# Kernel tuning notes

Hardware: AMD Instinct MI355X
Metric: run time of the kernel (lower is better)

The kernel has to match this reference:

```python
import jax, jax.numpy as jnp
import numpy as np

PAD = 1
K = 3  # kernel_size


def conv2d(x, w, b):
    y = jax.lax.conv_general_dilated(
        x, w, window_strides=(1, 1), padding=((PAD, PAD), (PAD, PAD)),
        dimension_numbers=("NCHW", "OIHW", "NCHW"))
    return y + b[None, :, None, None]


def deform_conv2d(x, offset, weight, bias):
    # torchvision.ops.deform_conv2d semantics (stride=1, dilation=1, 1 offset group)
    B, C, H, W = x.shape
    O = weight.shape[0]
    K2 = K * K
    off = offset.reshape(B, K2, 2, H, W)  # [...,0]=dy, [...,1]=dx
    ky, kx = jnp.meshgrid(jnp.arange(K), jnp.arange(K), indexing="ij")
    ky = ky.reshape(K2).astype(x.dtype)
    kx = kx.reshape(K2).astype(x.dtype)
    hh = jnp.arange(H, dtype=x.dtype)
    ww = jnp.arange(W, dtype=x.dtype)
    # sampling coords, shape [B, K2, H, W]
    py = off[:, :, 0] + ky[None, :, None, None] + hh[None, None, :, None] - PAD
    px = off[:, :, 1] + kx[None, :, None, None] + ww[None, None, None, :] - PAD

    y0 = jnp.floor(py)
    x0 = jnp.floor(px)
    wy = (py - y0)[:, None]  # [B,1,K2,H,W]
    wx = (px - x0)[:, None]

    xf = x.reshape(B, C, H * W)

    def gather(iy, ix):
        valid = (iy >= 0) & (iy < H) & (ix >= 0) & (ix < W)
        iyc = jnp.clip(iy, 0, H - 1).astype(jnp.int32)
        ixc = jnp.clip(ix, 0, W - 1).astype(jnp.int32)
        idx = (iyc * W + ixc).reshape(B, 1, K2 * H * W)
        v = jnp.take_along_axis(xf, idx, axis=2).reshape(B, C, K2, H, W)
        return v * valid.reshape(B, 1, K2, H, W).astype(x.dtype)

    v00 = gather(y0, x0)
    v01 = gather(y0, x0 + 1)
    v10 = gather(y0 + 1, x0)
    v11 = gather(y0 + 1, x0 + 1)
    sampled = (v00 * (1 - wy) * (1 - wx) + v01 * (1 - wy) * wx
               + v10 * wy * (1 - wx) + v11 * wy * wx)  # [B,C,K2,H,W]
    out = jnp.einsum("bckhw,ock->bohw", sampled, weight.reshape(O, C, K2))
    return out + bias[None, :, None, None]


def setup_inputs() -> dict:
    key = jax.random.key(0)
    k1, k2, k3, k4, k5 = jax.random.split(key, 5)
    B, C, H, W = 4, 64, 192, 192
    O = 64
    x = jax.random.normal(k1, (B, C, H, W), dtype=jnp.float32)
    w_off = jax.random.normal(k2, (2 * K * K, C, K, K), dtype=jnp.float32) * 0.05
    b_off = jnp.zeros((2 * K * K,), dtype=jnp.float32)
    w_conv = jax.random.normal(k3, (O, C, K, K), dtype=jnp.float32) * (1.0 / np.sqrt(C * K * K))
    b_conv = jax.random.normal(k4, (O,), dtype=jnp.float32) * 0.01
    return {"x": x, "w_off": w_off, "b_off": b_off, "w_conv": w_conv, "b_conv": b_conv}


def reference(x, w_off, b_off, w_conv, b_conv):
    offset = conv2d(x, w_off, b_off)
    y = deform_conv2d(x, offset, w_conv, b_conv)
    return conv2d(y, w_conv, b_conv)  # module reuses self.conv on deform output
```

## Files before the change

### kernel.cpp

```cpp
#include <hip/hip_runtime.h>

constexpr int B = 4;
constexpr int C = 64;
constexpr int O = 64;
constexpr int OOFF = 18;
constexpr int H = 192;
constexpr int W = 192;

typedef __attribute__((ext_vector_type(8))) short short8;
typedef __attribute__((ext_vector_type(4))) float float4v;
typedef __attribute__((ext_vector_type(2))) float f32x2;
typedef __attribute__((ext_vector_type(2))) uint u32x2;
typedef __attribute__((ext_vector_type(2))) __bf16 bf16x2;

__device__ inline ushort f2bf(float f) {
  return __builtin_bit_cast(ushort, (__bf16)f);
}
__device__ inline uint pk2bf(float lo, float hi) {
  bf16x2 v;
  v.x = (__bf16)lo;
  v.y = (__bf16)hi;
  return __builtin_bit_cast(uint, v);
}
__device__ inline f32x2 upk(uint u) {
  u32x2 t;
  t.x = u << 16;
  t.y = u & 0xffff0000u;
  return __builtin_bit_cast(f32x2, t);
}

__global__ __launch_bounds__(256) void k_pre(const float* __restrict__ x,
                                             ushort* __restrict__ xtb,
                                             const float* __restrict__ w_conv,
                                             ushort* __restrict__ wBf,
                                             const float* __restrict__ w_off,
                                             ushort* __restrict__ wOf) {
  __shared__ float tile[64][17];
  const int bid = blockIdx.x;
  const int tid = threadIdx.x;
  if (bid < 9216) {
    const int w0 = (bid % 12) * 16;
    const int h = (bid / 12) % 192;
    const int b = bid / 2304;
    const int wl = tid & 15;
    const int c0 = tid >> 4;
#pragma unroll
    for (int r = 0; r < 4; ++r) {
      const int c = c0 + r * 16;
      tile[c][wl] = x[(((size_t)b * C + c) * H + h) * W + w0 + wl];
    }
    __syncthreads();
    const int c = tid & 63;
    const int qq = tid >> 6;
#pragma unroll
    for (int r = 0; r < 4; ++r) {
      const int wq = qq + r * 4;
      xtb[(((size_t)b * H + h) * W + w0 + wq) * C + c] = f2bf(tile[c][wq]);
    }
  } else if (bid < 9360) {
    const int i = (bid - 9216) * 256 + tid;
    const int j = i & 7;
    const int lane = (i >> 3) & 63;
    const int nt = (i >> 9) & 3;
    const int kstep = (i >> 11) & 1;
    const int kk = i >> 12;
    const int n = nt + 4 * (lane & 15);
    const int c = kstep * 32 + ((lane >> 4) & 3) * 8 + j;
    wBf[i] = f2bf(w_conv[((size_t)n * C + c) * 9 + kk]);
  } else {
    const int i = (bid - 9360) * 256 + tid;
    const int j = i & 7;
    const int lane = (i >> 3) & 63;
    const int nt = (i >> 9) & 1;
    const int ks = (i >> 10) & 1;
    const int kk = i >> 11;
    const int n = nt * 16 + (lane & 15);
    const int c = ks * 32 + ((lane >> 4) & 3) * 8 + j;
    wOf[i] = (n < OOFF) ? f2bf(w_off[((size_t)n * C + c) * 9 + kk]) : (ushort)0;
  }
}

__global__ __launch_bounds__(128) void k_fused(
    const ushort* __restrict__ xtb, const ushort* __restrict__ wOf,
    const float* __restrict__ b_off, const ushort* __restrict__ wBf,
    const float* __restrict__ b_conv, ushort* __restrict__ yt) {
  __shared__ ushort sA[2][2][64][8];
  __shared__ __align__(16) float offBuf[2][16][20];

  const int bid = blockIdx.x;
  const int xcd = bid & 7;
  const int s0 = bid >> 3;
  const int b = xcd >> 1;
  const int half = xcd & 1;
  const int th = s0 / 24;
  const int tw = s0 % 24;

  const int tid = threadIdx.x;
  const int wave = tid >> 6, lane = tid & 63;
  const int h0 = half * 96 + th * 4 + wave * 2;
  const int w0 = tw * 8;

  const int col = lane & 15, quad = lane >> 4;
  const int p = lane >> 2, qtr = lane & 3;
  const int prow = p >> 3, pcol = p & 7;
  const int h = h0 + prow, w = w0 + pcol;
  const int ks_w = qtr >> 1;
  const int q2 = (qtr & 1) * 2;

  {
    float4v oacc[2];
#pragma unroll
    for (int nt = 0; nt < 2; ++nt) oacc[nt] = (float4v){0.f, 0.f, 0.f, 0.f};

    short8 oafr[2][2];

    auto oload = [&](int kk, int pb) {
      const int ky = kk / 3, kx = kk % 3;
      const int hh = h0 + (col >> 3) + ky - 1;
      const int ww = w0 + (col & 7) + kx - 1;
      const bool ok = ((unsigned)hh < (unsigned)H) && ((unsigned)ww < (unsigned)W);
      const int hhc = min(max(hh, 0), H - 1);
      const int wwc = min(max(ww, 0), W - 1);
      const ushort* pa = xtb + (((size_t)b * H + hhc) * W + wwc) * C + quad * 8;
#pragma unroll
      for (int ks = 0; ks < 2; ++ks) {
        short8 v = (short8)0;
        if (ok) v = *(const short8*)(pa + ks * 32);
        oafr[pb][ks] = v;
      }
    };

    oload(0, 0);
#pragma unroll
    for (int kk = 0; kk < 9; ++kk) {
      const int pb = kk & 1;
      if (kk < 8) oload(kk + 1, pb ^ 1);
#pragma unroll
      for (int ks = 0; ks < 2; ++ks)
#pragma unroll
        for (int nt = 0; nt < 2; ++nt) {
          const short8 bw =
              *(const short8*)&wOf[((((size_t)kk * 2 + ks) * 2 + nt) * 64 + lane) * 8];
          oacc[nt] = __builtin_amdgcn_mfma_f32_16x16x32_bf16(oafr[pb][ks], bw, oacc[nt], 0, 0, 0);
        }
    }

#pragma unroll
    for (int nt = 0; nt < 2; ++nt) {
      const int oc = nt * 16 + col;
      if (oc < OOFF) {
        const float bias = b_off[oc];
#pragma unroll
        for (int r = 0; r < 4; ++r)
          offBuf[wave][quad * 4 + r][oc] = oacc[nt][r] + bias;
      }
    }
  }

  const ushort* xbase = xtb + (size_t)b * H * W * C;
  const uint qoff = (uint)qtr * 32u;
  const float hm1 = (float)(h - 1), wm1 = (float)(w - 1);

  uint offs[4];
  float4 awv;
  uint4 gA[4], gB[4];

  auto calc = [&](int kk) {
    const float2 ov = *(const float2*)&offBuf[wave][p][2 * kk];
    const int ky = kk / 3, kx = kk % 3;
    const float pyf = ov.x + hm1 + (float)ky;
    const float pxf = ov.y + wm1 + (float)kx;
    const float fy0 = floorf(pyf), fx0 = floorf(pxf);
    const float wy = pyf - fy0, wx = pxf - fx0;
    const int iy0 = (int)fy0, ix0 = (int)fx0;
    const int iy1 = iy0 + 1, ix1 = ix0 + 1;
    const bool vy0 = (unsigned)iy0 < (unsigned)H;
    const bool vy1 = (unsigned)iy1 < (unsigned)H;
    const bool vx0 = (unsigned)ix0 < (unsigned)W;
    const bool vx1 = (unsigned)ix1 < (unsigned)W;
    awv.x = (vy0 && vx0) ? (1.f - wy) * (1.f - wx) : 0.f;
    awv.y = (vy0 && vx1) ? (1.f - wy) * wx : 0.f;
    awv.z = (vy1 && vx0) ? wy * (1.f - wx) : 0.f;
    awv.w = (vy1 && vx1) ? wy * wx : 0.f;
    const int cy0 = min(max(iy0, 0), H - 1), cy1 = min(max(iy1, 0), H - 1);
    const int cx0 = min(max(ix0, 0), W - 1), cx1 = min(max(ix1, 0), W - 1);
    offs[0] = (uint)((cy0 * W + cx0) * (C * 2)) + qoff;
    offs[1] = (uint)((cy0 * W + cx1) * (C * 2)) + qoff;
    offs[2] = (uint)((cy1 * W + cx0) * (C * 2)) + qoff;
    offs[3] = (uint)((cy1 * W + cx1) * (C * 2)) + qoff;
  };

  auto loadAB = [&]() {
#pragma unroll
    for (int c = 0; c < 4; ++c)
      gA[c] = *(const uint4*)((const char*)xbase + offs[c]);
#pragma unroll
    for (int c = 0; c < 4; ++c)
      gB[c] = *(const uint4*)((const char*)xbase + offs[c] + 16u);
  };
  auto blend = [&](const uint4* g, uint* pk) {
    const f32x2 a00 = {awv.x, awv.x};
    const f32x2 a01 = {awv.y, awv.y};
    const f32x2 a10 = {awv.z, awv.z};
    const f32x2 a11 = {awv.w, awv.w};
#pragma unroll
    for (int i = 0; i < 4; ++i) {
      f32x2 sv = upk(g[0][i]) * a00 + upk(g[1][i]) * a01 + upk(g[2][i]) * a10 + upk(g[3][i]) * a11;
      pk[i] = pk2bf(sv.x, sv.y);
    }
  };

  float4v acc[4];
#pragma unroll
  for (int nt = 0; nt < 4; ++nt) acc[nt] = (float4v){0.f, 0.f, 0.f, 0.f};

  calc(0);
  loadAB();
#pragma unroll
  for (int kk = 0; kk < 9; ++kk) {
    uint pkA[4];
    blend(gA, pkA);
    *(uint4*)&sA[wave][ks_w][p | (q2 << 4)][0] = *(const uint4*)pkA;
    uint pkB[4];
    blend(gB, pkB);
    *(uint4*)&sA[wave][ks_w][p | ((q2 + 1) << 4)][0] = *(const uint4*)pkB;

    if (kk < 8) {
      calc(kk + 1);
      loadAB();
    }

#pragma unroll
    for (int ks = 0; ks < 2; ++ks) {
      const short8 a = *(const short8*)&sA[wave][ks][lane][0];
#pragma unroll
      for (int nt = 0; nt < 4; ++nt) {
        const short8 bb = *(const short8*)&wBf[((((size_t)kk * 2 + ks) * 4 + nt) * 64 + lane) * 8];
        acc[nt] = __builtin_amdgcn_mfma_f32_16x16x32_bf16(a, bb, acc[nt], 0, 0, 0);
      }
    }
  }

  float bias[4];
#pragma unroll
  for (int nt = 0; nt < 4; ++nt) bias[nt] = b_conv[4 * col + nt];
#pragma unroll
  for (int r = 0; r < 4; ++r) {
    const int pp = quad * 4 + r;
    const int hrow = h0 + (pp >> 3), wcol = w0 + (pp & 7);
    uint2 u;
    u.x = pk2bf(acc[0][r] + bias[0], acc[1][r] + bias[1]);
    u.y = pk2bf(acc[2][r] + bias[2], acc[3][r] + bias[3]);
    *(uint2*)&yt[((size_t)(b * H + hrow) * W + wcol) * C + 4 * col] = u;
  }
}

__global__ __launch_bounds__(128) void k_conv_main_mfma(
    const ushort* __restrict__ yt, const ushort* __restrict__ wBf,
    const float* __restrict__ b_conv, float* __restrict__ out) {
  const int w0 = blockIdx.x * 16;
  const int b = blockIdx.z;
  const int tid = threadIdx.x;
  const int wave = tid >> 6, lane = tid & 63;
  const int col = lane & 15, quad = lane >> 4;
  const int h = blockIdx.y * 2 + wave;

  float4v acc[4];
#pragma unroll
  for (int nt = 0; nt < 4; ++nt) acc[nt] = (float4v){0.f, 0.f, 0.f, 0.f};

  short8 afr[2][2];

  auto load = [&](int kk, int pb) {
    const int ky = kk / 3, kx = kk % 3;
    const int ww = w0 + col + kx - 1;
    const int hh = h + ky - 1;
    const bool ok = ((unsigned)ww < (unsigned)W) && ((unsigned)hh < (unsigned)H);
    const int wwc = min(max(ww, 0), W - 1);
    const int hhc = min(max(hh, 0), H - 1);
    const ushort* pa = yt + (((size_t)b * H + hhc) * W + wwc) * C + quad * 8;
#pragma unroll
    for (int ks = 0; ks < 2; ++ks) {
      short8 v = (short8)0;
      if (ok) v = *(const short8*)(pa + ks * 32);
      afr[pb][ks] = v;
    }
  };

  load(0, 0);
#pragma unroll
  for (int kk = 0; kk < 9; ++kk) {
    const int pb = kk & 1;
    if (kk < 8) load(kk + 1, pb ^ 1);
#pragma unroll
    for (int ks = 0; ks < 2; ++ks)
#pragma unroll
      for (int nt = 0; nt < 4; ++nt) {
        const short8 bb = *(const short8*)&wBf[((((size_t)kk * 2 + ks) * 4 + nt) * 64 + lane) * 8];
        acc[nt] = __builtin_amdgcn_mfma_f32_16x16x32_bf16(afr[pb][ks], bb, acc[nt], 0, 0, 0);
      }
  }

  float bias[4];
#pragma unroll
  for (int nt = 0; nt < 4; ++nt) bias[nt] = b_conv[4 * col + nt];
#pragma unroll
  for (int nt = 0; nt < 4; ++nt) {
    const int oc = 4 * col + nt;
    float4 v;
    v.x = acc[nt][0] + bias[nt];
    v.y = acc[nt][1] + bias[nt];
    v.z = acc[nt][2] + bias[nt];
    v.w = acc[nt][3] + bias[nt];
    *(float4*)&out[(((size_t)b * O + oc) * H + h) * W + w0 + quad * 4] = v;
  }
}

extern "C" void kernel_launch(void* const* d_in, const int* in_sizes, int n_in,
                              void* d_out, int out_size, void* d_ws, size_t ws_size,
                              hipStream_t stream) {
  const float* x = (const float*)d_in[0];
  const float* w_off = (const float*)d_in[1];
  const float* b_off = (const float*)d_in[2];
  const float* w_conv = (const float*)d_in[3];
  const float* b_conv = (const float*)d_in[4];
  float* out = (float*)d_out;

  ushort* xtb = (ushort*)d_ws;
  ushort* yt = xtb + (size_t)B * H * W * C;
  ushort* wBf = yt + (size_t)B * H * W * C;
  ushort* wOf = wBf + 36864;

  k_pre<<<dim3(9432), dim3(256), 0, stream>>>(x, xtb, w_conv, wBf, w_off, wOf);
  k_fused<<<dim3(4608), dim3(128), 0, stream>>>(xtb, wOf, b_off, wBf, b_conv, yt);
  k_conv_main_mfma<<<dim3(W / 16, H / 2, B), dim3(128), 0, stream>>>(yt, wBf, b_conv, out);
}
```

Before: 209.2 us.

## Register-block two output rows per wave in final conv and remap deform gather channels

The final conv kernel now computes two output rows per wave, so each weight fragment loaded into registers feeds two MFMAs instead of one. Weight fragments are prefetched into a double buffer alongside the activations, and blocks grow to 256 threads covering 8 rows. Separately, the deform gather changes which channel chunks each lane loads (16-byte stride, second load at +64), which changes how the sampled values are laid out in shared memory. The cost is higher register pressure from the doubled accumulators and the buffered B fragments.

```diff
diff --git a/kernel.cpp b/kernel.cpp
--- a/kernel.cpp
+++ b/kernel.cpp
@@ -104,8 +104,6 @@
   const int p = lane >> 2, qtr = lane & 3;
   const int prow = p >> 3, pcol = p & 7;
   const int h = h0 + prow, w = w0 + pcol;
-  const int ks_w = qtr >> 1;
-  const int q2 = (qtr & 1) * 2;
 
   {
     float4v oacc[2];
@@ -158,7 +156,7 @@
   }
 
   const ushort* xbase = xtb + (size_t)b * H * W * C;
-  const uint qoff = (uint)qtr * 32u;
+  const uint qoff = (uint)qtr * 16u;
   const float hm1 = (float)(h - 1), wm1 = (float)(w - 1);
 
   uint offs[4];
@@ -196,7 +194,7 @@
       gA[c] = *(const uint4*)((const char*)xbase + offs[c]);
 #pragma unroll
     for (int c = 0; c < 4; ++c)
-      gB[c] = *(const uint4*)((const char*)xbase + offs[c] + 16u);
+      gB[c] = *(const uint4*)((const char*)xbase + offs[c] + 64u);
   };
   auto blend = [&](const uint4* g, uint* pk) {
     const f32x2 a00 = {awv.x, awv.x};
@@ -220,10 +218,10 @@
   for (int kk = 0; kk < 9; ++kk) {
     uint pkA[4];
     blend(gA, pkA);
-    *(uint4*)&sA[wave][ks_w][p | (q2 << 4)][0] = *(const uint4*)pkA;
+    *(uint4*)&sA[wave][0][p | (qtr << 4)][0] = *(const uint4*)pkA;
     uint pkB[4];
     blend(gB, pkB);
-    *(uint4*)&sA[wave][ks_w][p | ((q2 + 1) << 4)][0] = *(const uint4*)pkB;
+    *(uint4*)&sA[wave][1][p | (qtr << 4)][0] = *(const uint4*)pkB;
 
     if (kk < 8) {
       calc(kk + 1);
@@ -255,7 +253,7 @@
   }
 }
 
-__global__ __launch_bounds__(128) void k_conv_main_mfma(
+__global__ __launch_bounds__(256) void k_conv_main_mfma(
     const ushort* __restrict__ yt, const ushort* __restrict__ wBf,
     const float* __restrict__ b_conv, float* __restrict__ out) {
   const int w0 = blockIdx.x * 16;
@@ -263,27 +261,39 @@
   const int tid = threadIdx.x;
   const int wave = tid >> 6, lane = tid & 63;
   const int col = lane & 15, quad = lane >> 4;
-  const int h = blockIdx.y * 2 + wave;
-
-  float4v acc[4];
-#pragma unroll
-  for (int nt = 0; nt < 4; ++nt) acc[nt] = (float4v){0.f, 0.f, 0.f, 0.f};
-
-  short8 afr[2][2];
+  const int h0 = blockIdx.y * 8 + wave * 2;
+
+  float4v acc[2][4];
+#pragma unroll
+  for (int mt = 0; mt < 2; ++mt)
+#pragma unroll
+    for (int nt = 0; nt < 4; ++nt) acc[mt][nt] = (float4v){0.f, 0.f, 0.f, 0.f};
+
+  short8 bfr[2][2][4];
+  short8 afr[2][2][2];
 
   auto load = [&](int kk, int pb) {
     const int ky = kk / 3, kx = kk % 3;
     const int ww = w0 + col + kx - 1;
-    const int hh = h + ky - 1;
-    const bool ok = ((unsigned)ww < (unsigned)W) && ((unsigned)hh < (unsigned)H);
+    const bool wok = (unsigned)ww < (unsigned)W;
     const int wwc = min(max(ww, 0), W - 1);
-    const int hhc = min(max(hh, 0), H - 1);
-    const ushort* pa = yt + (((size_t)b * H + hhc) * W + wwc) * C + quad * 8;
-#pragma unroll
-    for (int ks = 0; ks < 2; ++ks) {
-      short8 v = (short8)0;
-      if (ok) v = *(const short8*)(pa + ks * 32);
-      afr[pb][ks] = v;
+#pragma unroll
+    for (int ks = 0; ks < 2; ++ks)
+#pragma unroll
+      for (int nt = 0; nt < 4; ++nt)
+        bfr[pb][ks][nt] = *(const short8*)&wBf[((((size_t)kk * 2 + ks) * 4 + nt) * 64 + lane) * 8];
+#pragma unroll
+    for (int mt = 0; mt < 2; ++mt) {
+      const int hh = h0 + mt + ky - 1;
+      const bool ok = wok && ((unsigned)hh < (unsigned)H);
+      const int hhc = min(max(hh, 0), H - 1);
+      const ushort* pa = yt + (((size_t)b * H + hhc) * W + wwc) * C + quad * 8;
+#pragma unroll
+      for (int ks = 0; ks < 2; ++ks) {
+        short8 v = (short8)0;
+        if (ok) v = *(const short8*)(pa + ks * 32);
+        afr[pb][mt][ks] = v;
+      }
     }
   };
 
@@ -295,24 +305,29 @@
 #pragma unroll
     for (int ks = 0; ks < 2; ++ks)
 #pragma unroll
-      for (int nt = 0; nt < 4; ++nt) {
-        const short8 bb = *(const short8*)&wBf[((((size_t)kk * 2 + ks) * 4 + nt) * 64 + lane) * 8];
-        acc[nt] = __builtin_amdgcn_mfma_f32_16x16x32_bf16(afr[pb][ks], bb, acc[nt], 0, 0, 0);
-      }
+      for (int mt = 0; mt < 2; ++mt)
+#pragma unroll
+        for (int nt = 0; nt < 4; ++nt)
+          acc[mt][nt] = __builtin_amdgcn_mfma_f32_16x16x32_bf16(afr[pb][mt][ks], bfr[pb][ks][nt],
+                                                                acc[mt][nt], 0, 0, 0);
   }
 
   float bias[4];
 #pragma unroll
   for (int nt = 0; nt < 4; ++nt) bias[nt] = b_conv[4 * col + nt];
 #pragma unroll
-  for (int nt = 0; nt < 4; ++nt) {
-    const int oc = 4 * col + nt;
-    float4 v;
-    v.x = acc[nt][0] + bias[nt];
-    v.y = acc[nt][1] + bias[nt];
-    v.z = acc[nt][2] + bias[nt];
-    v.w = acc[nt][3] + bias[nt];
-    *(float4*)&out[(((size_t)b * O + oc) * H + h) * W + w0 + quad * 4] = v;
+  for (int mt = 0; mt < 2; ++mt) {
+    const int h = h0 + mt;
+#pragma unroll
+    for (int nt = 0; nt < 4; ++nt) {
+      const int oc = 4 * col + nt;
+      float4 v;
+      v.x = acc[mt][nt][0] + bias[nt];
+      v.y = acc[mt][nt][1] + bias[nt];
+      v.z = acc[mt][nt][2] + bias[nt];
+      v.w = acc[mt][nt][3] + bias[nt];
+      *(float4*)&out[(((size_t)b * O + oc) * H + h) * W + w0 + quad * 4] = v;
+    }
   }
 }
 
@@ -333,5 +348,5 @@
 
   k_pre<<<dim3(9432), dim3(256), 0, stream>>>(x, xtb, w_conv, wBf, w_off, wOf);
   k_fused<<<dim3(4608), dim3(128), 0, stream>>>(xtb, wOf, b_off, wBf, b_conv, yt);
-  k_conv_main_mfma<<<dim3(W / 16, H / 2, B), dim3(128), 0, stream>>>(yt, wBf, b_conv, out);
-}
+  k_conv_main_mfma<<<dim3(W / 16, H / 8, B), dim3(256), 0, stream>>>(yt, wBf, b_conv, out);
+}
```

Measured after the change: 200.1 us. 1.05x faster.
